# Performance work log

Measured on AMD Instinct MI355X. Metric: run time of the kernel, lower is better.

Reference implementation:

```python
import jax, jax.numpy as jnp
import numpy as np

RF, US, MGC, FS, NS, NL = 1024, 200, 60, 64, 4, 10  # receptive field, upsample, mgc, filters, stacks, wavenet layers
SCALE = 0.70710678118


def setup_inputs() -> dict:
    key = jax.random.key(0)
    ks = jax.random.split(key, 16)
    F = 8
    N = F * US
    def n(k, shape, s=0.05):
        return jax.random.normal(k, shape, dtype=jnp.float32) * s
    return {
        "mgc": n(ks[0], (F, MGC), 1.0),
        "noise": n(ks[1], (N + RF,), 1.0),
        "cond_w": n(ks[2], (MGC * US, MGC)),          # conditioning Linear(60 -> 12000)
        "cond_b": n(ks[3], (MGC * US,)),
        "conv0_w": n(ks[4], (NS, 3, FS, 1, 2), 0.3),    # layer 0: in_ch=1, [input,gate,residual]
        "convs_w": n(ks[5], (NS, NL - 1, 3, FS, FS, 2), 0.08),
        "conv_b": n(ks[6], (NS, NL, 3, FS)),
        "ccw": n(ks[7], (NS, NL, 2, FS, MGC)),          # cond_input / cond_gate linear weights
        "ccb": n(ks[8], (NS, NL, 2, FS)),
        "pre_w": n(ks[9], (NS, 256, FS)),
        "pre_b": n(ks[10], (NS, 256)),
        "mean_w": n(ks[11], (NS, 1, 256)),
        "mean_b": n(ks[12], (NS, 1)),
        "std_w": n(ks[13], (NS, 1, 256)),
        "std_b": n(ks[14], (NS, 1)),
    }


def _cond_conv(x, cond, w, b, cw, cb):
    # x: [N, C, L]; kernel-2 stride-2 conv expressed as a reshape + einsum
    Nb, C, L = x.shape
    xr = x.reshape(Nb, C, L // 2, 2)
    inp = jnp.einsum('ncls,ocs->nol', xr, w[0]) + b[0][None, :, None]
    gate = jnp.einsum('ncls,ocs->nol', xr, w[1]) + b[1][None, :, None]
    res = jnp.einsum('ncls,ocs->nol', xr, w[2]) + b[2][None, :, None]
    ic = (cond @ cw[0].T + cb[0])[:, :, None]
    gc = (cond @ cw[1].T + cb[1])[:, :, None]
    return (jnp.tanh(inp + ic) * jax.nn.sigmoid(gate + gc) + res) * SCALE


def reference(mgc, noise, cond_w, cond_b, conv0_w, convs_w, conv_b, ccw, ccb,
              pre_w, pre_b, mean_w, mean_b, std_w, std_b):
    F = mgc.shape[0]
    N = F * US
    # conditioning: Linear(60 -> 60*200) + tanh, reshaped to one 60-dim vector per sample
    cond = jnp.tanh(mgc @ cond_w.T + cond_b).reshape(N, MGC)
    prepend = noise[:RF]
    prev_x = noise
    win_idx = jnp.arange(N)[:, None] + jnp.arange(RF)[None, :]  # strided-window gather
    tails = []
    mean = logvar = None
    for s in range(NS):
        x = prev_x[win_idx][:, None, :]  # [N, 1, RF]
        for l in range(NL):
            w = conv0_w[s] if l == 0 else convs_w[s, l - 1]
            x = _cond_conv(x, cond, w, conv_b[s, l], ccw[s, l], ccb[s, l])
        pre = jax.nn.relu(x[:, :, 0] @ pre_w[s].T + pre_b[s])   # [N, 256]
        mean = pre @ mean_w[s].T + mean_b[s]                    # [N, 1]
        logvar = pre @ std_w[s].T + std_b[s]                    # [N, 1]
        eps = prev_x[RF:].reshape(N, 1)
        new = eps * jnp.exp(0.5 * logvar) + mean
        tails.append(jax.lax.stop_gradient(new[-RF:]))
        if s != NS - 1:
            prev_x = jnp.concatenate([prepend, new.reshape(-1)])
        else:
            prev_x = new
    return prev_x, mean, logvar, jnp.stack(tails)
```

## Files before the change

kernel.cpp:

```cpp
#include <hip/hip_runtime.h>
#include <hip/hip_fp16.h>

#define RF    1024
#define USZ   200
#define NWIN  1600
#define SCALEF 0.70710678118f
#define TPB   512
#define CSTR  72

typedef _Float16 f16x8 __attribute__((ext_vector_type(8)));
typedef float    f32x4 __attribute__((ext_vector_type(4)));

#if __has_builtin(__builtin_amdgcn_exp2f)
#define EXP2F(x) __builtin_amdgcn_exp2f(x)
#else
#define EXP2F(x) exp2f(x)
#endif
#if __has_builtin(__builtin_amdgcn_rcpf)
#define RCPF(x) __builtin_amdgcn_rcpf(x)
#else
#define RCPF(x) (1.0f / (x))
#endif

__device__ __forceinline__ float gatecomb(float a, float g, float r) {
  a = fminf(a, 12.0f);
  g = fminf(g, 12.0f);
  const float u = EXP2F(a * 2.885390082f);
  const float v = EXP2F(g * 1.442695041f);
  const float d = RCPF((u + 1.0f) * (v + 1.0f));
  return fmaf((u - 1.0f) * v, d, r) * SCALEF;
}


__global__ void k_cond(const float* __restrict__ mgc, const float* __restrict__ cond_w,
                       const float* __restrict__ cond_b, float* __restrict__ cond) {
  int idx = blockIdx.x * 256 + threadIdx.x;
  int n = idx / 60, c = idx % 60;
  int u = n % USZ, f = n / USZ;
  float a = cond_b[u * 60 + c];
  const float* wr = cond_w + (u * 60 + c) * 60;
  const float* mr = mgc + f * 60;
#pragma unroll 10
  for (int m = 0; m < 60; ++m) a = fmaf(mr[m], wr[m], a);
  float e = EXP2F(a * 2.885390082f);
  cond[idx] = (e - 1.0f) * RCPF(e + 1.0f);
}

__global__ void k_icgc2(const float* __restrict__ cond, const float* __restrict__ ccw,
                        const float* __restrict__ ccb, const float* __restrict__ conv_b,
                        float* __restrict__ icgc) {
  __shared__ float lc[32 * 60];
  const int sl = blockIdx.y;
  const int n0 = blockIdx.x * 32;
  const int tid = threadIdx.x;
  for (int i = tid; i < 1920; i += 256) lc[i] = cond[n0 * 60 + i];
  __syncthreads();
  const int jo = tid & 127;
  const int nh = tid >> 7;
  const int j = jo >> 6, o = jo & 63;
  float w[60];
  const float* cw = ccw + ((sl * 2 + j) * 64 + o) * 60;
#pragma unroll
  for (int c = 0; c < 60; ++c) w[c] = cw[c];
  const float b = ccb[(sl * 2 + j) * 64 + o] + conv_b[(sl * 3 + j) * 64 + o];
  for (int nl = nh * 16; nl < nh * 16 + 16; ++nl) {
    float a = b;
    const float4* lc4 = (const float4*)(lc + nl * 60);
#pragma unroll
    for (int c4 = 0; c4 < 15; ++c4) {
      const float4 cv = lc4[c4];
      a = fmaf(cv.x, w[c4 * 4 + 0], a);
      a = fmaf(cv.y, w[c4 * 4 + 1], a);
      a = fmaf(cv.z, w[c4 * 4 + 2], a);
      a = fmaf(cv.w, w[c4 * 4 + 3], a);
    }
    icgc[((size_t)sl * 1600 + n0 + nl) * 128 + jo] = a;
  }
}

__global__ void k_wcvt(const float* __restrict__ convs_w, _Float16* __restrict__ wfrag) {
  int idx = blockIdx.x * 256 + threadIdx.x;
  int j    = idx & 7;
  int lane = (idx >> 3) & 63;
  int ks   = (idx >> 9) & 3;
  int ch16 = (idx >> 11) & 3;
  int t    = idx >> 13;
  int gate = t % 3, sl = t / 3;
  int o  = ch16 * 16 + (lane & 15);
  int kk = ks * 32 + (lane >> 4) * 8 + j;
  int s2 = kk >> 6, c = kk & 63;
  wfrag[idx] = (_Float16)convs_w[(((sl * 3 + gate) * 64 + o) * 64 + c) * 2 + s2];
}

__global__ void k_pwt(const float* __restrict__ pre_w, float* __restrict__ pwT) {
  int idx = blockIdx.x * 256 + threadIdx.x;
  int k = idx & 255, o = (idx >> 8) & 63, s = idx >> 14;
  pwT[idx] = pre_w[(s * 256 + k) * 64 + o];
}

__global__ void k_prefix(const float* __restrict__ noise, float* __restrict__ pxA,
                         float* __restrict__ pxB) {
  int i = blockIdx.x * 256 + threadIdx.x;
  float v = noise[i];
  pxA[i] = v; pxB[i] = v;
}

#define SMEM_BYTES 79184

__device__ __forceinline__ void run_mfma_tiles(
    const _Float16* __restrict__ ain, _Float16* __restrict__ aout, float* __restrict__ x64f,
    const f16x8 bfr[3][4], float bi, float bg, float br,
    int mt_lo, int mt_hi, int row_sub, int Lout, bool last,
    int q, int m16, int och)
{
  for (int mt = mt_lo; mt < mt_hi; mt += 2) {
    f32x4 ai = {bi, bi, bi, bi};
    f32x4 ag = {bg, bg, bg, bg};
    f32x4 ar = {br, br, br, br};
#pragma unroll
    for (int ks = 0; ks < 4; ++ks) {
      const int row = 2 * (mt * 16 + m16) + (ks >> 1) - row_sub;
      const f16x8 af = *(const f16x8*)(ain + row * CSTR + (ks & 1) * 32 + q * 8);
      ai = __builtin_amdgcn_mfma_f32_16x16x32_f16(af, bfr[0][ks], ai, 0, 0, 0);
      ag = __builtin_amdgcn_mfma_f32_16x16x32_f16(af, bfr[1][ks], ag, 0, 0, 0);
      ar = __builtin_amdgcn_mfma_f32_16x16x32_f16(af, bfr[2][ks], ar, 0, 0, 0);
    }
#pragma unroll
    for (int r = 0; r < 4; ++r) {
      const int p = mt * 16 + q * 4 + r;
      const float val = gatecomb(ai[r], ag[r], ar[r]);
      if (last) { if (p == 0) x64f[och] = val; }
      else if (p < Lout) aout[p * CSTR + och] = (_Float16)val;
    }
  }
}

__launch_bounds__(TPB, 4)
__global__ void k_window(int s, const float* __restrict__ px, float* __restrict__ ptail,
                         float* __restrict__ out,
                         const float* __restrict__ icgc, const float* __restrict__ conv_b,
                         const float* __restrict__ conv0_w, const _Float16* __restrict__ wfrag,
                         const float* __restrict__ pwT, const float* __restrict__ pre_b,
                         const float* __restrict__ mean_w, const float* __restrict__ mean_b,
                         const float* __restrict__ std_w, const float* __restrict__ std_b) {
  extern __shared__ char smem[];
  _Float16* bufA = (_Float16*)smem;
  _Float16* bufB = (_Float16*)(smem + 36864);
  float*    xw   = (float*)(smem + 73728);
  float*    x64f = (float*)(smem + 77840);
  float*    pre  = (float*)(smem + 78096);
  float*    red  = (float*)(smem + 79120);

  const int n = blockIdx.x;
  const int tid = threadIdx.x;
  const int wave = tid >> 6, lane = tid & 63;
  const int q = lane >> 4, m16 = lane & 15;
  const int ch16 = wave & 3, mstart = wave >> 2;
  const int och = ch16 * 16 + m16;

  for (int i = tid; i < 1025; i += TPB) xw[i] = px[n + i];

  const int b0 = ((s * 10 + 0) * 1600 + n) * 128;
  const float l0bi = icgc[b0 + lane];
  const float l0bg = icgc[b0 + 64 + lane];
  const float l0br = conv_b[((s * 10 + 0) * 3 + 2) * 64 + lane];
  const float wi0 = conv0_w[((s * 3 + 0) * 64 + lane) * 2 + 0];
  const float wi1 = conv0_w[((s * 3 + 0) * 64 + lane) * 2 + 1];
  const float wg0 = conv0_w[((s * 3 + 1) * 64 + lane) * 2 + 0];
  const float wg1 = conv0_w[((s * 3 + 1) * 64 + lane) * 2 + 1];
  const float wr0 = conv0_w[((s * 3 + 2) * 64 + lane) * 2 + 0];
  const float wr1 = conv0_w[((s * 3 + 2) * 64 + lane) * 2 + 1];

  f16x8 bfr1[3][4];
  {
    const f16x8* wb = (const f16x8*)(wfrag + (size_t)(s * 9) * 24576);
#pragma unroll
    for (int g = 0; g < 3; ++g)
#pragma unroll
      for (int ks = 0; ks < 4; ++ks)
        bfr1[g][ks] = wb[(((g * 4 + ch16) * 4 + ks) << 6) + lane];
  }
  const int base1 = ((s * 10 + 1) * 1600 + n) * 128;
  const float bi1 = icgc[base1 + och];
  const float bg1 = icgc[base1 + 64 + och];
  const float br1 = conv_b[((s * 10 + 1) * 3 + 2) * 64 + och];

  __syncthreads();

#pragma unroll 1
  for (int p = wave; p < 256; p += 8) {
    const float x0 = xw[2 * p], x1 = xw[2 * p + 1];
    const float vi = fmaf(x1, wi1, fmaf(x0, wi0, l0bi));
    const float vg = fmaf(x1, wg1, fmaf(x0, wg0, l0bg));
    const float vr = fmaf(x1, wr1, fmaf(x0, wr0, l0br));
    bufA[p * CSTR + lane] = (_Float16)gatecomb(vi, vg, vr);
  }
  __syncthreads();

  run_mfma_tiles(bufA, bufB, x64f, bfr1, bi1, bg1, br1, mstart, 8, 0, 256, false, q, m16, och);
  __syncthreads();

#pragma unroll 1
  for (int p = wave; p < 256; p += 8) {
    const int pg = 256 + p;
    const float x0 = xw[2 * pg], x1 = xw[2 * pg + 1];
    const float vi = fmaf(x1, wi1, fmaf(x0, wi0, l0bi));
    const float vg = fmaf(x1, wg1, fmaf(x0, wg0, l0bg));
    const float vr = fmaf(x1, wr1, fmaf(x0, wr0, l0br));
    bufA[p * CSTR + lane] = (_Float16)gatecomb(vi, vg, vr);
  }
  __syncthreads();

  run_mfma_tiles(bufA, bufB, x64f, bfr1, bi1, bg1, br1, 8 + mstart, 16, 256, 256, false, q, m16, och);
  __syncthreads();

  for (int l = 2; l <= 9; ++l) {
    const int Lout = 512 >> l;
    const int mtiles = (Lout + 15) >> 4;
    const _Float16* ain = (l & 1) ? bufA : bufB;
    _Float16* aout      = (l & 1) ? bufB : bufA;
    f16x8 bfr[3][4];
    const f16x8* wb = (const f16x8*)(wfrag + (size_t)(s * 9 + (l - 1)) * 24576);
#pragma unroll
    for (int g = 0; g < 3; ++g)
#pragma unroll
      for (int ks = 0; ks < 4; ++ks)
        bfr[g][ks] = wb[(((g * 4 + ch16) * 4 + ks) << 6) + lane];
    const int base = ((s * 10 + l) * 1600 + n) * 128;
    run_mfma_tiles(ain, aout, x64f, bfr,
                   icgc[base + och], icgc[base + 64 + och],
                   conv_b[((s * 10 + l) * 3 + 2) * 64 + och],
                   mstart, mtiles, 0, Lout, l == 9, q, m16, och);
    __syncthreads();
  }

  if (tid < 256) {
    const int k = tid;
    float a = pre_b[s * 256 + k];
#pragma unroll 8
    for (int oo = 0; oo < 64; ++oo)
      a = fmaf(x64f[oo], pwT[(s * 64 + oo) * 256 + k], a);
    pre[k] = fmaxf(a, 0.0f);
  }
  __syncthreads();
  {
    float pm = 0.0f, pv = 0.0f;
    if (tid < 256) {
      float pk = pre[tid];
      pm = pk * mean_w[s * 256 + tid];
      pv = pk * std_w[s * 256 + tid];
    }
    for (int off = 32; off >= 1; off >>= 1) {
      pm += __shfl_down(pm, off, 64);
      pv += __shfl_down(pv, off, 64);
    }
    if (lane == 0) { red[wave] = pm; red[8 + wave] = pv; }
  }
  __syncthreads();
  if (tid == 0) {
    float m = mean_b[s], lv = std_b[s];
#pragma unroll
    for (int w2 = 0; w2 < 8; ++w2) { m += red[w2]; lv += red[8 + w2]; }
    float eps = xw[1024];
    float nv = eps * __expf(0.5f * lv) + m;
    if (s == 3) { out[n] = nv; out[1600 + n] = m; out[3200 + n] = lv; }
    else ptail[n] = nv;
    if (n >= 576) out[4800 + s * 1024 + (n - 576)] = nv;
  }
}

extern "C" void kernel_launch(void* const* d_in, const int* in_sizes, int n_in,
                              void* d_out, int out_size, void* d_ws, size_t ws_size,
                              hipStream_t stream) {
  (void)in_sizes; (void)n_in; (void)out_size; (void)ws_size;
  const float* mgc     = (const float*)d_in[0];
  const float* noise   = (const float*)d_in[1];
  const float* cond_w  = (const float*)d_in[2];
  const float* cond_b  = (const float*)d_in[3];
  const float* conv0_w = (const float*)d_in[4];
  const float* convs_w = (const float*)d_in[5];
  const float* conv_b  = (const float*)d_in[6];
  const float* ccw     = (const float*)d_in[7];
  const float* ccb     = (const float*)d_in[8];
  const float* pre_w   = (const float*)d_in[9];
  const float* pre_b   = (const float*)d_in[10];
  const float* mean_w  = (const float*)d_in[11];
  const float* mean_b  = (const float*)d_in[12];
  const float* std_w   = (const float*)d_in[13];
  const float* std_b   = (const float*)d_in[14];
  float* out = (float*)d_out;

  float* ws_f = (float*)d_ws;
  float*    cond  = ws_f;
  float*    icgc  = cond + 96000;
  float*    pxA   = icgc + 8192000;
  float*    pxB   = pxA + 2624;
  float*    pwT   = pxB + 2624;
  _Float16* wfrag = (_Float16*)(pwT + 65536);

  k_cond<<<375, 256, 0, stream>>>(mgc, cond_w, cond_b, cond);
  k_icgc2<<<dim3(50, 40), 256, 0, stream>>>(cond, ccw, ccb, conv_b, icgc);
  k_wcvt<<<3456, 256, 0, stream>>>(convs_w, wfrag);
  k_pwt<<<256, 256, 0, stream>>>(pre_w, pwT);
  k_prefix<<<4, 256, 0, stream>>>(noise, pxA, pxB);

  (void)hipFuncSetAttribute((const void*)k_window,
                            hipFuncAttributeMaxDynamicSharedMemorySize, SMEM_BYTES);

  for (int s = 0; s < 4; ++s) {
    const float* pin = (s == 0) ? noise : (s == 1 ? pxA : (s == 2 ? pxB : pxA));
    float* pt = (s == 0) ? (pxA + 1024) : (s == 1 ? (pxB + 1024) : (s == 2 ? (pxA + 1024) : nullptr));
    k_window<<<NWIN, TPB, SMEM_BYTES, stream>>>(s, pin, pt, out, icgc, conv_b, conv0_w,
                                                wfrag, pwT, pre_b, mean_w, mean_b, std_w, std_b);
  }
}
```

Baseline: 664.5 us.

## Use MFMA for conditioning projections and double window block to 1024 threads

The conditioning projection kernel (icgc) is rewritten to use f16 MFMA on cond padded to 64 channels, with a new packing kernel that lays out ccw as B fragments. Separately, the main window kernel moves from 512 to 1024 threads per block (16 waves), with the tile loop stride and reduction slots adjusted to match. The aim is to cut the scalar FMA cost of the conditioning precompute and to raise wave-level parallelism per window. In exchange, the conditioning path loses precision through fp16, and register pressure rises under the new launch bounds.

New measurement: 1.915 ms. 188% more time.

```diff
diff --git a/kernel.cpp b/kernel.cpp
--- a/kernel.cpp
+++ b/kernel.cpp
@@ -5,7 +5,7 @@
 #define USZ   200
 #define NWIN  1600
 #define SCALEF 0.70710678118f
-#define TPB   512
+#define TPB   1024
 #define CSTR  72
 
 typedef _Float16 f16x8 __attribute__((ext_vector_type(8)));
@@ -33,9 +33,10 @@
 
 
 __global__ void k_cond(const float* __restrict__ mgc, const float* __restrict__ cond_w,
-                       const float* __restrict__ cond_b, float* __restrict__ cond) {
+                       const float* __restrict__ cond_b, _Float16* __restrict__ cond_h) {
   int idx = blockIdx.x * 256 + threadIdx.x;
-  int n = idx / 60, c = idx % 60;
+  int n = idx >> 6, c = idx & 63;
+  if (c >= 60) { cond_h[idx] = (_Float16)0.0f; return; }
   int u = n % USZ, f = n / USZ;
   float a = cond_b[u * 60 + c];
   const float* wr = cond_w + (u * 60 + c) * 60;
@@ -43,38 +44,50 @@
 #pragma unroll 10
   for (int m = 0; m < 60; ++m) a = fmaf(mr[m], wr[m], a);
   float e = EXP2F(a * 2.885390082f);
-  cond[idx] = (e - 1.0f) * RCPF(e + 1.0f);
-}
-
-__global__ void k_icgc2(const float* __restrict__ cond, const float* __restrict__ ccw,
-                        const float* __restrict__ ccb, const float* __restrict__ conv_b,
-                        float* __restrict__ icgc) {
-  __shared__ float lc[32 * 60];
+  cond_h[idx] = (_Float16)((e - 1.0f) * RCPF(e + 1.0f));
+}
+
+__global__ void k_packB(const float* __restrict__ ccw, _Float16* __restrict__ wfrag2) {
+  int idx = blockIdx.x * 256 + threadIdx.x;
+  int j    = idx & 7;
+  int lane = (idx >> 3) & 63;
+  int ks   = (idx >> 9) & 1;
+  int nt   = (idx >> 10) & 7;
+  int sl   = idx >> 13;
+  int jo = nt * 16 + (lane & 15);
+  int c  = ks * 32 + (lane >> 4) * 8 + j;
+  float v = 0.0f;
+  if (c < 60) v = ccw[((sl * 2 + (jo >> 6)) * 64 + (jo & 63)) * 60 + c];
+  wfrag2[idx] = (_Float16)v;
+}
+
+__global__ void k_icgc_mfma(const _Float16* __restrict__ cond_h, const _Float16* __restrict__ wfrag2,
+                            const float* __restrict__ ccb, const float* __restrict__ conv_b,
+                            float* __restrict__ icgc) {
+  const int n0 = blockIdx.x * 32;
   const int sl = blockIdx.y;
-  const int n0 = blockIdx.x * 32;
   const int tid = threadIdx.x;
-  for (int i = tid; i < 1920; i += 256) lc[i] = cond[n0 * 60 + i];
-  __syncthreads();
-  const int jo = tid & 127;
-  const int nh = tid >> 7;
-  const int j = jo >> 6, o = jo & 63;
-  float w[60];
-  const float* cw = ccw + ((sl * 2 + j) * 64 + o) * 60;
-#pragma unroll
-  for (int c = 0; c < 60; ++c) w[c] = cw[c];
-  const float b = ccb[(sl * 2 + j) * 64 + o] + conv_b[(sl * 3 + j) * 64 + o];
-  for (int nl = nh * 16; nl < nh * 16 + 16; ++nl) {
-    float a = b;
-    const float4* lc4 = (const float4*)(lc + nl * 60);
-#pragma unroll
-    for (int c4 = 0; c4 < 15; ++c4) {
-      const float4 cv = lc4[c4];
-      a = fmaf(cv.x, w[c4 * 4 + 0], a);
-      a = fmaf(cv.y, w[c4 * 4 + 1], a);
-      a = fmaf(cv.z, w[c4 * 4 + 2], a);
-      a = fmaf(cv.w, w[c4 * 4 + 3], a);
-    }
-    icgc[((size_t)sl * 1600 + n0 + nl) * 128 + jo] = a;
+  const int wave = tid >> 6, lane = tid & 63;
+  const int m16 = lane & 15, q = lane >> 4;
+  for (int t = wave; t < 16; t += 4) {
+    const int mt = t >> 3, nt = t & 7;
+    const int jo = nt * 16 + m16;
+    const float b = ccb[(sl * 2 + (jo >> 6)) * 64 + (jo & 63)]
+                  + conv_b[(sl * 3 + (jo >> 6)) * 64 + (jo & 63)];
+    f32x4 acc = {b, b, b, b};
+    const int arow = (n0 + mt * 16 + m16) * 64 + q * 8;
+    const f16x8 a0 = *(const f16x8*)(cond_h + arow);
+    const f16x8 a1 = *(const f16x8*)(cond_h + arow + 32);
+    const f16x8* wb = (const f16x8*)wfrag2;
+    const f16x8 b0 = wb[(((sl * 8 + nt) * 2 + 0) << 6) + lane];
+    const f16x8 b1 = wb[(((sl * 8 + nt) * 2 + 1) << 6) + lane];
+    acc = __builtin_amdgcn_mfma_f32_16x16x32_f16(a0, b0, acc, 0, 0, 0);
+    acc = __builtin_amdgcn_mfma_f32_16x16x32_f16(a1, b1, acc, 0, 0, 0);
+#pragma unroll
+    for (int r = 0; r < 4; ++r) {
+      const int n = n0 + mt * 16 + q * 4 + r;
+      icgc[((size_t)sl * 1600 + n) * 128 + jo] = acc[r];
+    }
   }
 }
 
@@ -105,7 +118,16 @@
   pxA[i] = v; pxB[i] = v;
 }
 
-#define SMEM_BYTES 79184
+#define SMEM_BYTES 79248
+
+__device__ __forceinline__ void load_bfr(f16x8 bfr[3][4], const f16x8* __restrict__ wb,
+                                         int ch16, int lane) {
+#pragma unroll
+  for (int g = 0; g < 3; ++g)
+#pragma unroll
+    for (int ks = 0; ks < 4; ++ks)
+      bfr[g][ks] = wb[(((g * 4 + ch16) * 4 + ks) << 6) + lane];
+}
 
 __device__ __forceinline__ void run_mfma_tiles(
     const _Float16* __restrict__ ain, _Float16* __restrict__ aout, float* __restrict__ x64f,
@@ -113,7 +135,7 @@
     int mt_lo, int mt_hi, int row_sub, int Lout, bool last,
     int q, int m16, int och)
 {
-  for (int mt = mt_lo; mt < mt_hi; mt += 2) {
+  for (int mt = mt_lo; mt < mt_hi; mt += 4) {
     f32x4 ai = {bi, bi, bi, bi};
     f32x4 ag = {bg, bg, bg, bg};
     f32x4 ar = {br, br, br, br};
@@ -135,7 +157,33 @@
   }
 }
 
-__launch_bounds__(TPB, 4)
+__device__ __forceinline__ void do_l0_chunk(
+    const float* __restrict__ xw, _Float16* __restrict__ bufA,
+    const float* __restrict__ icgc, const float* __restrict__ conv_b,
+    const float* __restrict__ conv0_w, int s, int n, int wave, int lane, int pbase)
+{
+  const int b0 = ((s * 10 + 0) * 1600 + n) * 128;
+  const float l0bi = icgc[b0 + lane];
+  const float l0bg = icgc[b0 + 64 + lane];
+  const float l0br = conv_b[((s * 10 + 0) * 3 + 2) * 64 + lane];
+  const float wi0 = conv0_w[((s * 3 + 0) * 64 + lane) * 2 + 0];
+  const float wi1 = conv0_w[((s * 3 + 0) * 64 + lane) * 2 + 1];
+  const float wg0 = conv0_w[((s * 3 + 1) * 64 + lane) * 2 + 0];
+  const float wg1 = conv0_w[((s * 3 + 1) * 64 + lane) * 2 + 1];
+  const float wr0 = conv0_w[((s * 3 + 2) * 64 + lane) * 2 + 0];
+  const float wr1 = conv0_w[((s * 3 + 2) * 64 + lane) * 2 + 1];
+#pragma unroll 1
+  for (int p = wave; p < 256; p += 16) {
+    const int pg = pbase + p;
+    const float x0 = xw[2 * pg], x1 = xw[2 * pg + 1];
+    const float vi = fmaf(x1, wi1, fmaf(x0, wi0, l0bi));
+    const float vg = fmaf(x1, wg1, fmaf(x0, wg0, l0bg));
+    const float vr = fmaf(x1, wr1, fmaf(x0, wr0, l0br));
+    bufA[p * CSTR + lane] = (_Float16)gatecomb(vi, vg, vr);
+  }
+}
+
+__launch_bounds__(TPB, 8)
 __global__ void k_window(int s, const float* __restrict__ px, float* __restrict__ ptail,
                          float* __restrict__ out,
                          const float* __restrict__ icgc, const float* __restrict__ conv_b,
@@ -159,59 +207,32 @@
   const int och = ch16 * 16 + m16;
 
   for (int i = tid; i < 1025; i += TPB) xw[i] = px[n + i];
-
-  const int b0 = ((s * 10 + 0) * 1600 + n) * 128;
-  const float l0bi = icgc[b0 + lane];
-  const float l0bg = icgc[b0 + 64 + lane];
-  const float l0br = conv_b[((s * 10 + 0) * 3 + 2) * 64 + lane];
-  const float wi0 = conv0_w[((s * 3 + 0) * 64 + lane) * 2 + 0];
-  const float wi1 = conv0_w[((s * 3 + 0) * 64 + lane) * 2 + 1];
-  const float wg0 = conv0_w[((s * 3 + 1) * 64 + lane) * 2 + 0];
-  const float wg1 = conv0_w[((s * 3 + 1) * 64 + lane) * 2 + 1];
-  const float wr0 = conv0_w[((s * 3 + 2) * 64 + lane) * 2 + 0];
-  const float wr1 = conv0_w[((s * 3 + 2) * 64 + lane) * 2 + 1];
-
-  f16x8 bfr1[3][4];
+  __syncthreads();
+
+  do_l0_chunk(xw, bufA, icgc, conv_b, conv0_w, s, n, wave, lane, 0);
+  __syncthreads();
+
   {
-    const f16x8* wb = (const f16x8*)(wfrag + (size_t)(s * 9) * 24576);
-#pragma unroll
-    for (int g = 0; g < 3; ++g)
-#pragma unroll
-      for (int ks = 0; ks < 4; ++ks)
-        bfr1[g][ks] = wb[(((g * 4 + ch16) * 4 + ks) << 6) + lane];
-  }
-  const int base1 = ((s * 10 + 1) * 1600 + n) * 128;
-  const float bi1 = icgc[base1 + och];
-  const float bg1 = icgc[base1 + 64 + och];
-  const float br1 = conv_b[((s * 10 + 1) * 3 + 2) * 64 + och];
-
-  __syncthreads();
-
-#pragma unroll 1
-  for (int p = wave; p < 256; p += 8) {
-    const float x0 = xw[2 * p], x1 = xw[2 * p + 1];
-    const float vi = fmaf(x1, wi1, fmaf(x0, wi0, l0bi));
-    const float vg = fmaf(x1, wg1, fmaf(x0, wg0, l0bg));
-    const float vr = fmaf(x1, wr1, fmaf(x0, wr0, l0br));
-    bufA[p * CSTR + lane] = (_Float16)gatecomb(vi, vg, vr);
-  }
-  __syncthreads();
-
-  run_mfma_tiles(bufA, bufB, x64f, bfr1, bi1, bg1, br1, mstart, 8, 0, 256, false, q, m16, och);
-  __syncthreads();
-
-#pragma unroll 1
-  for (int p = wave; p < 256; p += 8) {
-    const int pg = 256 + p;
-    const float x0 = xw[2 * pg], x1 = xw[2 * pg + 1];
-    const float vi = fmaf(x1, wi1, fmaf(x0, wi0, l0bi));
-    const float vg = fmaf(x1, wg1, fmaf(x0, wg0, l0bg));
-    const float vr = fmaf(x1, wr1, fmaf(x0, wr0, l0br));
-    bufA[p * CSTR + lane] = (_Float16)gatecomb(vi, vg, vr);
-  }
-  __syncthreads();
-
-  run_mfma_tiles(bufA, bufB, x64f, bfr1, bi1, bg1, br1, 8 + mstart, 16, 256, 256, false, q, m16, och);
+    f16x8 bfr[3][4];
+    load_bfr(bfr, (const f16x8*)(wfrag + (size_t)(s * 9) * 24576), ch16, lane);
+    const int base1 = ((s * 10 + 1) * 1600 + n) * 128;
+    run_mfma_tiles(bufA, bufB, x64f, bfr, icgc[base1 + och], icgc[base1 + 64 + och],
+                   conv_b[((s * 10 + 1) * 3 + 2) * 64 + och],
+                   mstart, 8, 0, 256, false, q, m16, och);
+  }
+  __syncthreads();
+
+  do_l0_chunk(xw, bufA, icgc, conv_b, conv0_w, s, n, wave, lane, 256);
+  __syncthreads();
+
+  {
+    f16x8 bfr[3][4];
+    load_bfr(bfr, (const f16x8*)(wfrag + (size_t)(s * 9) * 24576), ch16, lane);
+    const int base1 = ((s * 10 + 1) * 1600 + n) * 128;
+    run_mfma_tiles(bufA, bufB, x64f, bfr, icgc[base1 + och], icgc[base1 + 64 + och],
+                   conv_b[((s * 10 + 1) * 3 + 2) * 64 + och],
+                   8 + mstart, 16, 256, 256, false, q, m16, och);
+  }
   __syncthreads();
 
   for (int l = 2; l <= 9; ++l) {
@@ -220,12 +241,7 @@
     const _Float16* ain = (l & 1) ? bufA : bufB;
     _Float16* aout      = (l & 1) ? bufB : bufA;
     f16x8 bfr[3][4];
-    const f16x8* wb = (const f16x8*)(wfrag + (size_t)(s * 9 + (l - 1)) * 24576);
-#pragma unroll
-    for (int g = 0; g < 3; ++g)
-#pragma unroll
-      for (int ks = 0; ks < 4; ++ks)
-        bfr[g][ks] = wb[(((g * 4 + ch16) * 4 + ks) << 6) + lane];
+    load_bfr(bfr, (const f16x8*)(wfrag + (size_t)(s * 9 + (l - 1)) * 24576), ch16, lane);
     const int base = ((s * 10 + l) * 1600 + n) * 128;
     run_mfma_tiles(ain, aout, x64f, bfr,
                    icgc[base + och], icgc[base + 64 + och],
@@ -254,13 +270,13 @@
       pm += __shfl_down(pm, off, 64);
       pv += __shfl_down(pv, off, 64);
     }
-    if (lane == 0) { red[wave] = pm; red[8 + wave] = pv; }
+    if (lane == 0) { red[wave] = pm; red[16 + wave] = pv; }
   }
   __syncthreads();
   if (tid == 0) {
     float m = mean_b[s], lv = std_b[s];
 #pragma unroll
-    for (int w2 = 0; w2 < 8; ++w2) { m += red[w2]; lv += red[8 + w2]; }
+    for (int w2 = 0; w2 < 16; ++w2) { m += red[w2]; lv += red[16 + w2]; }
     float eps = xw[1024];
     float nv = eps * __expf(0.5f * lv) + m;
     if (s == 3) { out[n] = nv; out[1600 + n] = m; out[3200 + n] = lv; }
@@ -290,16 +306,18 @@
   const float* std_b   = (const float*)d_in[14];
   float* out = (float*)d_out;
 
-  float* ws_f = (float*)d_ws;
-  float*    cond  = ws_f;
-  float*    icgc  = cond + 96000;
-  float*    pxA   = icgc + 8192000;
-  float*    pxB   = pxA + 2624;
-  float*    pwT   = pxB + 2624;
-  _Float16* wfrag = (_Float16*)(pwT + 65536);
-
-  k_cond<<<375, 256, 0, stream>>>(mgc, cond_w, cond_b, cond);
-  k_icgc2<<<dim3(50, 40), 256, 0, stream>>>(cond, ccw, ccb, conv_b, icgc);
+  char* ws = (char*)d_ws;
+  float*    icgc   = (float*)ws;
+  float*    pxA    = (float*)(ws + 32768000);
+  float*    pxB    = (float*)(ws + 32778496);
+  float*    pwT    = (float*)(ws + 32788992);
+  _Float16* wfrag  = (_Float16*)(ws + 33051136);
+  _Float16* wfrag2 = (_Float16*)(ws + 34820608);
+  _Float16* cond_h = (_Float16*)(ws + 35475968);
+
+  k_cond<<<400, 256, 0, stream>>>(mgc, cond_w, cond_b, cond_h);
+  k_packB<<<1280, 256, 0, stream>>>(ccw, wfrag2);
+  k_icgc_mfma<<<dim3(50, 40), 256, 0, stream>>>(cond_h, wfrag2, ccb, conv_b, icgc);
   k_wcvt<<<3456, 256, 0, stream>>>(convs_w, wfrag);
   k_pwt<<<256, 256, 0, stream>>>(pre_w, pwT);
   k_prefix<<<4, 256, 0, stream>>>(noise, pxA, pxB);
```
